# Kernel optimization log

Measured on AMD Instinct MI355X. Metric: run time of the kernel, lower is better.

Reference implementation:

```python
import jax, jax.numpy as jnp
import numpy as np

N, F, M, E = 8192, 256, 128, 131072


def setup_inputs() -> dict:
    key = jax.random.key(0)
    k = jax.random.split(key, 6)
    x = jax.random.normal(k[0], (N, F), dtype=jnp.float32)
    edge_index = jax.random.randint(k[1], (2, E), 0, N, dtype=jnp.int64)
    eps = jax.random.normal(k[2], (N, M), dtype=jnp.float32)
    # small init scale so sigmoid(z_i . z_j) isn't saturated
    W_mu = jax.random.normal(k[3], (F, M), dtype=jnp.float32) * 0.05
    b_mu = jnp.zeros((M,), dtype=jnp.float32)
    W_sig = jax.random.normal(k[4], (F, M), dtype=jnp.float32) * 0.05
    b_sig = jnp.zeros((M,), dtype=jnp.float32)
    return {"x": x, "edge_index": edge_index, "eps": eps,
            "W_mu": W_mu, "b_mu": b_mu, "W_sig": W_sig, "b_sig": b_sig}


def reference(x, edge_index, eps, W_mu, b_mu, W_sig, b_sig):
    # Gaussian encoder: Normal(mu, exp(logstd)), Independent over latent dim
    mu = x @ W_mu + b_mu                      # [N, M]
    logstd = x @ W_sig + b_sig                # [N, M]
    sigma = jnp.exp(logstd)
    z = mu + sigma * eps                      # rsample, [N, M]

    # decoder.probability(dot(z_i, z_j)) = sigmoid(logit); vectorized as Z @ Z.T
    logits = z @ z.T                          # [N, N]

    # symmetric adjacency labels from edge_index (either direction counts)
    src, dst = edge_index[0], edge_index[1]
    adj = jnp.zeros((N, N), dtype=jnp.float32)
    adj = adj.at[src, dst].set(1.0)
    adj = adj.at[dst, src].set(1.0)

    # BCE(sigmoid(s), y) summed over unordered pairs i < j (stable logits form)
    per_pair = jax.nn.softplus(logits) - adj * logits  # = -[y log p + (1-y) log(1-p)]
    triu = jnp.triu(jnp.ones((N, N), dtype=bool), k=1)
    bce = jnp.sum(jnp.where(triu, per_pair, 0.0))

    # sum_i KL( N(mu_i, sigma_i) || N(0, I) )
    kl = jnp.sum(0.5 * (sigma * sigma + mu * mu - 1.0) - logstd)

    return bce + 0.001 * kl
```

## Files before the change

### kernel.cpp

```cpp
#include <hip/hip_runtime.h>

#define NN 8192
#define FF 256
#define MM 128
#define HSLOTS 262144

typedef __attribute__((ext_vector_type(8))) short bf16x8;
typedef __attribute__((ext_vector_type(4))) float f32x4;

#define P_KL    0
#define P_EDGE  (64 * 16)
#define P_SP    (128 * 16)
#define Z_OFF   16384
#define Z_BYTES (NN * MM * 2)
#define HASH_OFF (Z_OFF + Z_BYTES)
#define WT_OFF  (HASH_OFF + HSLOTS * 4)
#define WT_BYTES (MM * FF * 2)
#define ZF_OFF  (WT_OFF + 2 * WT_BYTES)

__device__ __forceinline__ float wave_reduce(float v) {
    #pragma unroll
    for (int off = 32; off > 0; off >>= 1) v += __shfl_down(v, off);
    return v;
}
__device__ __forceinline__ unsigned short f2bf(float f) {
    unsigned int u = __float_as_uint(f);
    u += 0x7fffu + ((u >> 16) & 1u);
    return (unsigned short)(u >> 16);
}
__device__ __forceinline__ int4 pack8(float4 a, float4 b) {
    int4 p;
    p.x = (int)f2bf(a.x) | ((int)f2bf(a.y) << 16);
    p.y = (int)f2bf(a.z) | ((int)f2bf(a.w) << 16);
    p.z = (int)f2bf(b.x) | ((int)f2bf(b.y) << 16);
    p.w = (int)f2bf(b.z) | ((int)f2bf(b.w) << 16);
    return p;
}

__global__ __launch_bounds__(256)
void prep_w(const float* __restrict__ Wmu, const float* __restrict__ Wsg,
            unsigned short* __restrict__ WmuT, unsigned short* __restrict__ WsgT,
            float* __restrict__ part, unsigned int* __restrict__ ht) {
    const int t = blockIdx.x * 256 + threadIdx.x;
    const int n = t >> 8, f = t & 255;
    WmuT[t] = f2bf(Wmu[f * MM + n]);
    WsgT[t] = f2bf(Wsg[f * MM + n]);
    if (t < 4096) part[t] = 0.f;
    uint4 z4 = {0u, 0u, 0u, 0u};
    ((uint4*)ht)[t * 2]     = z4;
    ((uint4*)ht)[t * 2 + 1] = z4;
}

#define XP_I4 33
#define XP_S  264

__global__ __launch_bounds__(256)
void encoder_mfma(const float* __restrict__ x, const float* __restrict__ eps,
                  const unsigned short* __restrict__ WmuT,
                  const unsigned short* __restrict__ WsgT,
                  const float* __restrict__ bmu, const float* __restrict__ bsg,
                  unsigned short* __restrict__ zb, float* __restrict__ part) {
    __shared__ int4 ax[16 * XP_I4];
    __shared__ float red[4];
    const int tid = threadIdx.x;
    const int wid = tid >> 6, lane = tid & 63;
    const int l15 = lane & 15, quad = lane >> 4;
    const int row0 = blockIdx.x * 16;

    {
        const int r = tid >> 4, ch = tid & 15;
        const float4* g0 = (const float4*)(x + (size_t)(row0 + r) * FF + ch * 8);
        const float4* g1 = (const float4*)(x + (size_t)(row0 + r) * FF + (ch + 16) * 8);
        ax[r * XP_I4 + ch]      = pack8(g0[0], g0[1]);
        ax[r * XP_I4 + ch + 16] = pack8(g1[0], g1[1]);
    }
    __syncthreads();

    const short* sax = (const short*)ax;
    const int4* wtm = (const int4*)WmuT;
    const int4* wts = (const int4*)WsgT;

    f32x4 zero4 = {0.f, 0.f, 0.f, 0.f};
    f32x4 accm[2], accl[2];
    accm[0] = accm[1] = accl[0] = accl[1] = zero4;

    #pragma unroll
    for (int ks = 0; ks < 8; ++ks) {
        const bf16x8 a = *(const bf16x8*)&sax[l15 * XP_S + ks * 32 + quad * 8];
        #pragma unroll
        for (int j = 0; j < 2; ++j) {
            const int n = wid * 32 + j * 16 + l15;
            const bf16x8 bmf = *(const bf16x8*)&wtm[n * 32 + ks * 4 + quad];
            const bf16x8 bsf = *(const bf16x8*)&wts[n * 32 + ks * 4 + quad];
            accm[j] = __builtin_amdgcn_mfma_f32_16x16x32_bf16(a, bmf, accm[j], 0, 0, 0);
            accl[j] = __builtin_amdgcn_mfma_f32_16x16x32_bf16(a, bsf, accl[j], 0, 0, 0);
        }
    }

    float klp = 0.f;
    #pragma unroll
    for (int j = 0; j < 2; ++j) {
        const int col = wid * 32 + j * 16 + l15;
        const float bm = bmu[col], bs = bsg[col];
        #pragma unroll
        for (int r = 0; r < 4; ++r) {
            const int row = row0 + quad * 4 + r;
            const float mu = accm[j][r] + bm;
            const float ls = accl[j][r] + bs;
            const float sg = __expf(ls);
            const float zz = fmaf(sg, eps[(size_t)row * MM + col], mu);
            zb[(size_t)row * MM + col] = f2bf(zz);
            klp += 0.5f * (sg * sg + mu * mu - 1.f) - ls;
        }
    }

    klp = wave_reduce(klp);
    if (lane == 0) red[wid] = klp;
    __syncthreads();
    if (tid == 0)
        atomicAdd(&part[P_KL + (blockIdx.x & 63) * 16],
                  red[0] + red[1] + red[2] + red[3]);
}

__global__ __launch_bounds__(256)
void zf_shuffle(const unsigned short* __restrict__ zb,
                unsigned short* __restrict__ zf) {
    const int t = blockIdx.x * 256 + threadIdx.x;
    const int rt = t >> 8, kq = (t >> 4) & 15, l15 = t & 15;
    const int4 v = *(const int4*)(zb + ((size_t)(rt * 16 + l15) * MM + kq * 8));
    ((int4*)zf)[t] = v;
}

__device__ __forceinline__ float dotpair(unsigned int a, unsigned int b) {
    const float al = __uint_as_float(a << 16);
    const float ah = __uint_as_float(a & 0xffff0000u);
    const float bl = __uint_as_float(b << 16);
    const float bh = __uint_as_float(b & 0xffff0000u);
    return fmaf(al, bl, ah * bh);
}

__global__ __launch_bounds__(256)
void edge_kernel(const int* __restrict__ ei, int E,
                 const unsigned short* __restrict__ zb,
                 unsigned int* __restrict__ ht, float* __restrict__ part) {
    const int tid = threadIdx.x;
    const int wid = tid >> 6, lane = tid & 63;
    const int g = lane >> 4, l15 = lane & 15;
    const int base0 = blockIdx.x * 128 + wid * 32;

    float accum = 0.f;
    #pragma unroll 2
    for (int p = 0; p < 8; ++p) {
        const int e = base0 + p * 4 + g;
        float s = 0.f;
        int i = 0, j = 0, a = 0, b = 0;
        if (e < E) {
            i = ei[e];
            j = ei[E + e];
            a = min(i, j); b = max(i, j);
            const uint4 ua = ((const uint4*)(zb + (size_t)a * MM))[l15];
            const uint4 ub = ((const uint4*)(zb + (size_t)b * MM))[l15];
            s = dotpair(ua.x, ub.x) + dotpair(ua.y, ub.y)
              + dotpair(ua.z, ub.z) + dotpair(ua.w, ub.w);
        }
        s += __shfl_down(s, 8);
        s += __shfl_down(s, 4);
        s += __shfl_down(s, 2);
        s += __shfl_down(s, 1);
        if (l15 == 0 && e < E && i != j) {
            const unsigned int key = (unsigned int)a * NN + b;
            unsigned int slot = (key * 2654435761u) & (HSLOTS - 1);
            bool first = false;
            for (;;) {
                const unsigned int old = atomicCAS(&ht[slot], 0u, key);
                if (old == 0u) { first = true; break; }
                if (old == key) break;
                slot = (slot + 1) & (HSLOTS - 1);
            }
            if (first) accum += s;
        }
    }
    accum = wave_reduce(accum);
    if (lane == 0)
        atomicAdd(&part[P_EDGE + ((blockIdx.x * 4 + wid) & 63) * 16], accum);
}

__global__ __launch_bounds__(256)
void tile_kernel(const unsigned short* __restrict__ zf, float* __restrict__ part) {
    const int q = blockIdx.x;
    int bi = (int)((129.0f - sqrtf(fmaxf(129.0f * 129.0f - 8.0f * (float)q, 0.f))) * 0.5f);
    bi = max(0, min(bi, 63));
    while ((bi + 1) * (129 - (bi + 1)) / 2 <= q && bi < 63) ++bi;
    while (bi * (129 - bi) / 2 > q) --bi;
    const int bj = bi + (q - bi * (129 - bi) / 2);

    const int tid = threadIdx.x;
    const int wid = tid >> 6, lane = tid & 63;
    const int wm = wid >> 1, wn = wid & 1;
    const int l15 = lane & 15, quad = lane >> 4;

    const bf16x8* zv = (const bf16x8*)zf;
    const int art = bi * 8 + wm * 4;
    const int brt = bj * 8 + wn * 4;

    f32x4 zero4 = {0.f, 0.f, 0.f, 0.f};
    f32x4 acc[4][4];
    #pragma unroll
    for (int i = 0; i < 4; ++i)
        #pragma unroll
        for (int j = 0; j < 4; ++j) acc[i][j] = zero4;

    bf16x8 aA[4], bA[4], aB[4], bB[4];
    #define LOADF(dstA, dstB, ks)                                             \
        _Pragma("unroll")                                                     \
        for (int t = 0; t < 4; ++t) {                                         \
            dstA[t] = zv[((art + t) * 16 + (ks) * 4 + quad) * 16 + l15];      \
            dstB[t] = zv[((brt + t) * 16 + (ks) * 4 + quad) * 16 + l15];      \
        }
    #define MFMAS(srcA, srcB)                                                 \
        _Pragma("unroll")                                                     \
        for (int i = 0; i < 4; ++i)                                           \
            _Pragma("unroll")                                                 \
            for (int j = 0; j < 4; ++j)                                       \
                acc[i][j] = __builtin_amdgcn_mfma_f32_16x16x32_bf16(          \
                    srcA[i], srcB[j], acc[i][j], 0, 0, 0);

    LOADF(aA, bA, 0)
    LOADF(aB, bB, 1)
    MFMAS(aA, bA)
    LOADF(aA, bA, 2)
    MFMAS(aB, bB)
    LOADF(aB, bB, 3)
    MFMAS(aA, bA)
    MFMAS(aB, bB)
    #undef LOADF
    #undef MFMAS

    float tsum = 0.f;
    if (bi != bj) {
        #pragma unroll
        for (int i = 0; i < 4; ++i)
            #pragma unroll
            for (int j = 0; j < 4; ++j)
                #pragma unroll
                for (int r = 0; r < 4; ++r) {
                    const float v = acc[i][j][r];
                    const float e = __expf(-fabsf(v));
                    tsum += fmaxf(v, 0.f) + e * fmaf(e, -0.5f, 1.f);
                }
    } else {
        const int rbase = wm * 64 + quad * 4;
        const int cbase = wn * 64 + l15;
        #pragma unroll
        for (int i = 0; i < 4; ++i)
            #pragma unroll
            for (int j = 0; j < 4; ++j)
                #pragma unroll
                for (int r = 0; r < 4; ++r)
                    if (cbase + j * 16 > rbase + i * 16 + r) {
                        const float v = acc[i][j][r];
                        const float e = __expf(-fabsf(v));
                        tsum += fmaxf(v, 0.f) + e * fmaf(e, -0.5f, 1.f);
                    }
    }

    tsum = wave_reduce(tsum);
    if (lane == 0)
        atomicAdd(&part[P_SP + ((q * 4 + wid) & 63) * 16], tsum);
}

__global__ void combine_kernel(const float* __restrict__ part,
                               float* __restrict__ out) {
    const int t = threadIdx.x;
    float v = part[P_SP + t * 16] - part[P_EDGE + t * 16]
            + 0.001f * part[P_KL + t * 16];
    v = wave_reduce(v);
    if (t == 0) out[0] = v;
}

extern "C" void kernel_launch(void* const* d_in, const int* in_sizes, int n_in,
                              void* d_out, int out_size, void* d_ws, size_t ws_size,
                              hipStream_t stream) {
    const float* x   = (const float*)d_in[0];
    const int* ei    = (const int*)d_in[1];
    const float* eps = (const float*)d_in[2];
    const float* Wmu = (const float*)d_in[3];
    const float* bmu = (const float*)d_in[4];
    const float* Wsg = (const float*)d_in[5];
    const float* bsg = (const float*)d_in[6];
    float* out = (float*)d_out;
    char* ws = (char*)d_ws;

    float* part = (float*)ws;
    unsigned short* zb = (unsigned short*)(ws + Z_OFF);
    unsigned int* ht = (unsigned int*)(ws + HASH_OFF);
    unsigned short* WmuT = (unsigned short*)(ws + WT_OFF);
    unsigned short* WsgT = (unsigned short*)(ws + WT_OFF + WT_BYTES);
    unsigned short* zf = (unsigned short*)(ws + ZF_OFF);
    const int E = in_sizes[1] / 2;

    prep_w<<<128, 256, 0, stream>>>(Wmu, Wsg, WmuT, WsgT, part, ht);
    encoder_mfma<<<NN / 16, 256, 0, stream>>>(x, eps, WmuT, WsgT, bmu, bsg, zb, part);
    zf_shuffle<<<512, 256, 0, stream>>>(zb, zf);
    edge_kernel<<<(E + 127) / 128, 256, 0, stream>>>(ei, E, zb, ht, part);
    tile_kernel<<<2080, 256, 0, stream>>>(zf, part);
    combine_kernel<<<1, 64, 0, stream>>>(part, out);
}
```

Measured before the change: 134.6 us.

## Fold zf shuffle into encoder and merge edge and tile kernels

```diff
diff --git a/kernel.cpp b/kernel.cpp
--- a/kernel.cpp
+++ b/kernel.cpp
@@ -59,7 +59,8 @@
                   const unsigned short* __restrict__ WmuT,
                   const unsigned short* __restrict__ WsgT,
                   const float* __restrict__ bmu, const float* __restrict__ bsg,
-                  unsigned short* __restrict__ zb, float* __restrict__ part) {
+                  unsigned short* __restrict__ zb, unsigned short* __restrict__ zf,
+                  float* __restrict__ part) {
     __shared__ int4 ax[16 * XP_I4];
     __shared__ float red[4];
     const int tid = threadIdx.x;
@@ -97,11 +98,13 @@
         }
     }
 
+    const int rt = row0 >> 4;
     float klp = 0.f;
     #pragma unroll
     for (int j = 0; j < 2; ++j) {
         const int col = wid * 32 + j * 16 + l15;
         const float bm = bmu[col], bs = bsg[col];
+        const int kq = col >> 3, c7 = col & 7;
         #pragma unroll
         for (int r = 0; r < 4; ++r) {
             const int row = row0 + quad * 4 + r;
@@ -109,7 +112,9 @@
             const float ls = accl[j][r] + bs;
             const float sg = __expf(ls);
             const float zz = fmaf(sg, eps[(size_t)row * MM + col], mu);
-            zb[(size_t)row * MM + col] = f2bf(zz);
+            const unsigned short zv = f2bf(zz);
+            zb[(size_t)row * MM + col] = zv;
+            zf[(size_t)(((rt * 16 + kq) * 16) + quad * 4 + r) * 8 + c7] = zv;
             klp += 0.5f * (sg * sg + mu * mu - 1.f) - ls;
         }
     }
@@ -122,15 +127,6 @@
                   red[0] + red[1] + red[2] + red[3]);
 }
 
-__global__ __launch_bounds__(256)
-void zf_shuffle(const unsigned short* __restrict__ zb,
-                unsigned short* __restrict__ zf) {
-    const int t = blockIdx.x * 256 + threadIdx.x;
-    const int rt = t >> 8, kq = (t >> 4) & 15, l15 = t & 15;
-    const int4 v = *(const int4*)(zb + ((size_t)(rt * 16 + l15) * MM + kq * 8));
-    ((int4*)zf)[t] = v;
-}
-
 __device__ __forceinline__ float dotpair(unsigned int a, unsigned int b) {
     const float al = __uint_as_float(a << 16);
     const float ah = __uint_as_float(a & 0xffff0000u);
@@ -140,65 +136,63 @@
 }
 
 __global__ __launch_bounds__(256)
-void edge_kernel(const int* __restrict__ ei, int E,
-                 const unsigned short* __restrict__ zb,
-                 unsigned int* __restrict__ ht, float* __restrict__ part) {
+void fused_kernel(const int* __restrict__ ei, int E, int eblocks,
+                  const unsigned short* __restrict__ zb,
+                  const unsigned short* __restrict__ zf,
+                  unsigned int* __restrict__ ht, float* __restrict__ part) {
     const int tid = threadIdx.x;
     const int wid = tid >> 6, lane = tid & 63;
-    const int g = lane >> 4, l15 = lane & 15;
-    const int base0 = blockIdx.x * 128 + wid * 32;
-
-    float accum = 0.f;
-    #pragma unroll 2
-    for (int p = 0; p < 8; ++p) {
-        const int e = base0 + p * 4 + g;
-        float s = 0.f;
-        int i = 0, j = 0, a = 0, b = 0;
-        if (e < E) {
-            i = ei[e];
-            j = ei[E + e];
-            a = min(i, j); b = max(i, j);
-            const uint4 ua = ((const uint4*)(zb + (size_t)a * MM))[l15];
-            const uint4 ub = ((const uint4*)(zb + (size_t)b * MM))[l15];
-            s = dotpair(ua.x, ub.x) + dotpair(ua.y, ub.y)
-              + dotpair(ua.z, ub.z) + dotpair(ua.w, ub.w);
+    const int l15 = lane & 15, quad = lane >> 4;
+
+    if ((int)blockIdx.x < eblocks) {
+        const int g = lane >> 4;
+        const int base0 = blockIdx.x * 128 + wid * 32;
+        float accum = 0.f;
+        #pragma unroll 2
+        for (int p = 0; p < 8; ++p) {
+            const int e = base0 + p * 4 + g;
+            float s = 0.f;
+            int i = 0, j = 0, a = 0, b = 0;
+            if (e < E) {
+                i = ei[e];
+                j = ei[E + e];
+                a = min(i, j); b = max(i, j);
+                const uint4 ua = ((const uint4*)(zb + (size_t)a * MM))[l15];
+                const uint4 ub = ((const uint4*)(zb + (size_t)b * MM))[l15];
+                s = dotpair(ua.x, ub.x) + dotpair(ua.y, ub.y)
+                  + dotpair(ua.z, ub.z) + dotpair(ua.w, ub.w);
+            }
+            s += __shfl_down(s, 8);
+            s += __shfl_down(s, 4);
+            s += __shfl_down(s, 2);
+            s += __shfl_down(s, 1);
+            if (l15 == 0 && e < E && i != j) {
+                const unsigned int key = (unsigned int)a * NN + b;
+                unsigned int slot = (key * 2654435761u) & (HSLOTS - 1);
+                bool first = false;
+                for (;;) {
+                    const unsigned int old = atomicCAS(&ht[slot], 0u, key);
+                    if (old == 0u) { first = true; break; }
+                    if (old == key) break;
+                    slot = (slot + 1) & (HSLOTS - 1);
+                }
+                if (first) accum += s;
+            }
         }
-        s += __shfl_down(s, 8);
-        s += __shfl_down(s, 4);
-        s += __shfl_down(s, 2);
-        s += __shfl_down(s, 1);
-        if (l15 == 0 && e < E && i != j) {
-            const unsigned int key = (unsigned int)a * NN + b;
-            unsigned int slot = (key * 2654435761u) & (HSLOTS - 1);
-            bool first = false;
-            for (;;) {
-                const unsigned int old = atomicCAS(&ht[slot], 0u, key);
-                if (old == 0u) { first = true; break; }
-                if (old == key) break;
-                slot = (slot + 1) & (HSLOTS - 1);
-            }
-            if (first) accum += s;
-        }
-    }
-    accum = wave_reduce(accum);
-    if (lane == 0)
-        atomicAdd(&part[P_EDGE + ((blockIdx.x * 4 + wid) & 63) * 16], accum);
-}
-
-__global__ __launch_bounds__(256)
-void tile_kernel(const unsigned short* __restrict__ zf, float* __restrict__ part) {
-    const int q = blockIdx.x;
+        accum = wave_reduce(accum);
+        if (lane == 0)
+            atomicAdd(&part[P_EDGE + ((blockIdx.x * 4 + wid) & 63) * 16], accum);
+        return;
+    }
+
+    const int q = blockIdx.x - eblocks;
     int bi = (int)((129.0f - sqrtf(fmaxf(129.0f * 129.0f - 8.0f * (float)q, 0.f))) * 0.5f);
     bi = max(0, min(bi, 63));
     while ((bi + 1) * (129 - (bi + 1)) / 2 <= q && bi < 63) ++bi;
     while (bi * (129 - bi) / 2 > q) --bi;
     const int bj = bi + (q - bi * (129 - bi) / 2);
 
-    const int tid = threadIdx.x;
-    const int wid = tid >> 6, lane = tid & 63;
     const int wm = wid >> 1, wn = wid & 1;
-    const int l15 = lane & 15, quad = lane >> 4;
-
     const bf16x8* zv = (const bf16x8*)zf;
     const int art = bi * 8 + wm * 4;
     const int brt = bj * 8 + wn * 4;
@@ -298,11 +292,12 @@
     unsigned short* WsgT = (unsigned short*)(ws + WT_OFF + WT_BYTES);
     unsigned short* zf = (unsigned short*)(ws + ZF_OFF);
     const int E = in_sizes[1] / 2;
+    const int eblocks = (E + 127) / 128;
 
     prep_w<<<128, 256, 0, stream>>>(Wmu, Wsg, WmuT, WsgT, part, ht);
-    encoder_mfma<<<NN / 16, 256, 0, stream>>>(x, eps, WmuT, WsgT, bmu, bsg, zb, part);
-    zf_shuffle<<<512, 256, 0, stream>>>(zb, zf);
-    edge_kernel<<<(E + 127) / 128, 256, 0, stream>>>(ei, E, zb, ht, part);
-    tile_kernel<<<2080, 256, 0, stream>>>(zf, part);
+    encoder_mfma<<<NN / 16, 256, 0, stream>>>(x, eps, WmuT, WsgT, bmu, bsg,
+                                              zb, zf, part);
+    fused_kernel<<<eblocks + 2080, 256, 0, stream>>>(ei, E, eblocks, zb, zf,
+                                                     ht, part);
     combine_kernel<<<1, 64, 0, stream>>>(part, out);
 }
```

Measured after the change: 132.2 us. No clear change (-1.8%).
